# Kernel optimization log

Hardware: AMD Instinct MI355X
Metric: run time of the kernel (lower is better)

## Reference

```python
import jax, jax.numpy as jnp
import numpy as np
from jax import lax

H = 768            # encoder hidden size (bert-base)
NUM_LABELS = 3     # hardcoded in QNetwork.forward


def setup_inputs() -> dict:
    key = jax.random.key(0)
    ks = jax.random.split(key, 12)
    B, S1, S2 = 4, 256, 64
    s = 0.02
    f32 = jnp.float32
    return {
        "states": jax.random.normal(ks[0], (B, S1, H), f32),
        "state_mask": jnp.ones((B, S1), f32),
        "actions": jax.random.normal(ks[1], (B, S2, H), f32),
        "actions_mask": jnp.ones((B, S2), f32),
        # LSTM layer 0 (input h), layers 1-2 (input 2h); dirs stacked on axis 0
        "Wih0": jax.random.normal(ks[2], (2, 4 * H, H), f32) * s,
        "Whh0": jax.random.normal(ks[3], (2, 4 * H, H), f32) * s,
        "b0": jnp.zeros((2, 4 * H), f32),
        "Wih12": jax.random.normal(ks[4], (2, 2, 4 * H, 2 * H), f32) * s,
        "Whh12": jax.random.normal(ks[5], (2, 2, 4 * H, H), f32) * s,
        "b12": jnp.zeros((2, 2, 4 * H), f32),
        # AttentionLayer MLP: Linear(3h->h), ReLU, Linear(h->1)
        "attn_W1": jax.random.normal(ks[6], (H, 3 * H), f32) * s,
        "attn_b1": jnp.zeros((H,), f32),
        "attn_W2": jax.random.normal(ks[7], (1, H), f32) * s,
        "attn_b2": jnp.zeros((1,), f32),
        # dueling value head Linear(2h->1)
        "val_W": jax.random.normal(ks[8], (1, 2 * H), f32) * s,
        "val_b": jnp.zeros((1,), f32),
        # bilinear scoring weight [num_labels, h, 2h] and bias [num_labels]
        "weight": jax.random.normal(ks[9], (NUM_LABELS, H, 2 * H), f32) * s,
        "bias": jnp.zeros((NUM_LABELS,), f32),
    }


def _bilstm_layer(x, Wih, Whh, b):
    """x: [B,T,in]; Wih/Whh: [2,4h,*]; b: [2,4h] (b_ih+b_hh). Returns [B,T,2h]."""
    B = x.shape[0]
    Hh = Whh.shape[-1]
    xs = jnp.swapaxes(x, 0, 1)  # [T,B,in]
    outs = []
    for d, rev in ((0, False), (1, True)):
        Wi, Wh, bb = Wih[d], Whh[d], b[d]
        def step(carry, xt, Wi=Wi, Wh=Wh, bb=bb):
            h, c = carry
            g = xt @ Wi.T + h @ Wh.T + bb
            i, f, gg, o = jnp.split(g, 4, axis=-1)  # torch gate order i,f,g,o
            c = jax.nn.sigmoid(f) * c + jax.nn.sigmoid(i) * jnp.tanh(gg)
            h = jax.nn.sigmoid(o) * jnp.tanh(c)
            return (h, c), h
        init = (jnp.zeros((B, Hh), x.dtype), jnp.zeros((B, Hh), x.dtype))
        _, ys = lax.scan(step, init, xs, reverse=rev)
        outs.append(jnp.swapaxes(ys, 0, 1))
    return jnp.concatenate(outs, -1)


def _forward(states, state_mask, actions, actions_mask,
             Wih0, Whh0, b0, Wih12, Whh12, b12,
             attn_W1, attn_b1, attn_W2, attn_b2,
             val_W, val_b, weight, bias):
    # 3-layer bidirectional LSTM + tanh
    out = _bilstm_layer(states, Wih0, Whh0, b0)
    for l in range(2):
        out = _bilstm_layer(out, Wih12[l], Whh12[l], b12[l])
    out = jnp.tanh(out)  # [B,S1,2h]

    # AttentionLayer(query=actions, key=value=out, q_mask=actions_mask, k_mask=state_mask)
    # First linear on concat([q,k]) split into query/key parts to avoid materializing the 3h concat.
    W1q, W1k = attn_W1[:, :H], attn_W1[:, H:]
    hq = jnp.einsum('bqh,eh->bqe', actions, W1q)          # [B,S2,h]
    hk = jnp.einsum('bkh,eh->bke', out, W1k)              # [B,S1,h]
    h1 = jax.nn.relu(hq[:, :, None, :] + hk[:, None, :, :] + attn_b1)  # [B,S2,S1,h]
    scores = jnp.einsum('bqke,e->bqk', h1, attn_W2[0]) + attn_b2[0]    # [B,S2,S1]
    mask = actions_mask[:, :, None] * state_mask[:, None, :]
    A = jnp.exp(jnp.where(mask == 0, -jnp.inf, scores))
    A_sum = jnp.clip(jnp.sum(A, axis=-1, keepdims=True), 2e-15, None)
    states_feat = jnp.einsum('bqk,bkd->bqd', A / A_sum, out)  # [B,S2,2h]

    # masked mean over seq2 (aggregate='attn_mean')
    num = jnp.sum(actions_mask, axis=1)[:, None, None]
    state_semantic = jnp.sum(states_feat, axis=1, keepdims=True) / num  # [B,1,2h]

    # adv scores: sum_h actions[b,q,h] * (weight[l,h,d] states_feat[b,q,d])
    adv = jnp.einsum('lhd,bqd,bqh->bql', weight, states_feat, actions) + bias  # [B,S2,3]

    # dueling value head
    val = state_semantic @ val_W.T + val_b  # [B,1,1]
    q_value = val + adv - jnp.mean(adv, axis=(1, 2), keepdims=True)  # [B,S2,3]

    # actions_mask is all-ones so the nonzero-gather is the identity
    return q_value.reshape(-1, NUM_LABELS)


def reference(states, state_mask, actions, actions_mask,
              Wih0, Whh0, b0, Wih12, Whh12, b12,
              attn_W1, attn_b1, attn_W2, attn_b2,
              val_W, val_b, weight, bias):
    return _forward(states, state_mask, actions, actions_mask,
                    Wih0, Whh0, b0, Wih12, Whh12, b12,
                    attn_W1, attn_b1, attn_W2, attn_b2,
                    val_W, val_b, weight, bias)
```

## Files before the change

### kernel.cpp

```cpp
#include <hip/hip_runtime.h>

#define HD 768
#define G4 3072
#define T1 256
#define NS2 64
#define NL 3
#define NBLK_DIR 128
#define UPB 6

__device__ __forceinline__ float sigf(float x) { return 1.0f / (1.0f + expf(-x)); }

__device__ __forceinline__ void fence_vm() {
    asm volatile("s_waitcnt vmcnt(0)" ::: "memory");
}

__global__ __launch_bounds__(256) void gemm_f32(
    const float* __restrict__ A, int lda,
    const float* __restrict__ W, int ldw,
    const float* __restrict__ bias,
    float* __restrict__ C,
    int K, int n_per_chunk, long long chunk_stride)
{
    __shared__ __align__(16) float As[16 * 64];
    __shared__ __align__(16) float Ws[16 * 64];
    const int tid = threadIdx.x;
    const int tx = tid & 15, ty = tid >> 4;
    const int n0 = blockIdx.x * 64, m0 = blockIdx.y * 64;
    const int lr = tid >> 2, lc = tid & 3;

    float acc[4][4] = {{0.f}};
    const float* Ap = A + (size_t)(m0 + lr) * lda + lc * 4;
    const float* Wp = W + (size_t)(n0 + lr) * ldw + lc * 4;

    for (int k0 = 0; k0 < K; k0 += 16) {
        float4 av = *(const float4*)(Ap + k0);
        float4 wv = *(const float4*)(Wp + k0);
        __syncthreads();
        As[(lc * 4 + 0) * 64 + lr] = av.x;
        As[(lc * 4 + 1) * 64 + lr] = av.y;
        As[(lc * 4 + 2) * 64 + lr] = av.z;
        As[(lc * 4 + 3) * 64 + lr] = av.w;
        Ws[(lc * 4 + 0) * 64 + lr] = wv.x;
        Ws[(lc * 4 + 1) * 64 + lr] = wv.y;
        Ws[(lc * 4 + 2) * 64 + lr] = wv.z;
        Ws[(lc * 4 + 3) * 64 + lr] = wv.w;
        __syncthreads();
#pragma unroll
        for (int k = 0; k < 16; ++k) {
            float4 a = *(const float4*)&As[k * 64 + ty * 4];
            float4 b = *(const float4*)&Ws[k * 64 + tx * 4];
            float aa[4] = {a.x, a.y, a.z, a.w};
            float bb[4] = {b.x, b.y, b.z, b.w};
#pragma unroll
            for (int i = 0; i < 4; ++i)
#pragma unroll
                for (int j = 0; j < 4; ++j) acc[i][j] += aa[i] * bb[j];
        }
    }

    const int jg = n0 + tx * 4;
    const int chunk = jg / n_per_chunk;
    const int jo = jg - chunk * n_per_chunk;
    float4 bv = make_float4(0.f, 0.f, 0.f, 0.f);
    if (bias) bv = *(const float4*)&bias[jg];
    float* Cb = C + (size_t)chunk * chunk_stride + jo;
#pragma unroll
    for (int i = 0; i < 4; ++i) {
        const int m = m0 + ty * 4 + i;
        float4 o;
        o.x = acc[i][0] + bv.x;
        o.y = acc[i][1] + bv.y;
        o.z = acc[i][2] + bv.z;
        o.w = acc[i][3] + bv.w;
        *(float4*)&Cb[(size_t)m * n_per_chunk] = o;
    }
}

__global__ __launch_bounds__(256) void lstm_scan(
    const float* __restrict__ Whh,
    const float* __restrict__ G,
    float* __restrict__ Hout,
    float* __restrict__ hglob,
    unsigned* __restrict__ bar,
    int last)
{
    __shared__ __align__(16) float4 hs[960];
    __shared__ float gl[24 * 4];
    __shared__ float cst[24];
    const int tid = threadIdx.x;
    const int bid = blockIdx.x;
    const int dir = bid & 1;
    const int blkd = bid >> 1;
    const int u0 = blkd * UPB;

    const int ks = tid & 15, jp = tid >> 4;
    const bool act = (jp < 12);
    const bool kz = act && (ks == 0);

    const int r0 = 2 * jp, r1 = 2 * jp + 1;
    const int j0 = (r0 / 6) * HD + u0 + (r0 % 6);
    const int j1 = (r1 / 6) * HD + u0 + (r1 % 6);
    float4 w0[12], w1[12];
    if (act) {
        const float4* W4 = (const float4*)Whh + (size_t)dir * G4 * 192;
#pragma unroll
        for (int i = 0; i < 12; ++i) {
            w0[i] = W4[(size_t)j0 * 192 + i * 16 + ks];
            w1[i] = W4[(size_t)j1 * 192 + i * 16 + ks];
        }
    }
    if (tid < 24) cst[tid] = 0.f;

    unsigned* ctr = bar + dir * 256;
    unsigned* genp = bar + 512 + dir * 32;
    const size_t gdb = (size_t)dir * 4 * T1 * G4;
    const size_t bstr = (size_t)T1 * G4;
    float* hsf = (float*)hs;

    for (int s = 0; s < T1; ++s) {
        const int t = dir ? (T1 - 1 - s) : s;

        float gA[4], gB[4];
        if (kz) {
            const float* Gt = G + gdb + (size_t)t * G4;
#pragma unroll
            for (int b = 0; b < 4; ++b) {
                gA[b] = Gt[(size_t)b * bstr + j0];
                gB[b] = Gt[(size_t)b * bstr + j1];
            }
        }

        if (s == 0) {
#pragma unroll
            for (int r = 0; r < 3; ++r) {
                const int k = tid + 256 * r;
                hs[5 * (k >> 2) + (k & 3)] = make_float4(0.f, 0.f, 0.f, 0.f);
            }
        } else {
            const float* hp = hglob + ((size_t)((s & 1) * 2 + dir)) * HD * 4;
            float hv[12];
#pragma unroll
            for (int r = 0; r < 12; ++r)
                hv[r] = __hip_atomic_load(hp + tid + 256 * r, __ATOMIC_RELAXED,
                                          __HIP_MEMORY_SCOPE_AGENT);
#pragma unroll
            for (int r = 0; r < 12; ++r) {
                const int i = tid + 256 * r;
                const int k = i >> 2, b = i & 3;
                hsf[(5 * (k >> 2) + (k & 3)) * 4 + b] = hv[r];
            }
        }
        __syncthreads();

        if (act) {
            float4 a0 = make_float4(0.f, 0.f, 0.f, 0.f);
            float4 a1 = make_float4(0.f, 0.f, 0.f, 0.f);
#pragma unroll
            for (int i = 0; i < 12; ++i) {
                const int pb = 5 * (i * 16 + ks);
                const float4 h0 = hs[pb + 0];
                const float4 h1 = hs[pb + 1];
                const float4 h2 = hs[pb + 2];
                const float4 h3 = hs[pb + 3];
                const float4 wa = w0[i];
                const float4 wb = w1[i];
                a0.x += wa.x * h0.x; a0.y += wa.x * h0.y; a0.z += wa.x * h0.z; a0.w += wa.x * h0.w;
                a0.x += wa.y * h1.x; a0.y += wa.y * h1.y; a0.z += wa.y * h1.z; a0.w += wa.y * h1.w;
                a0.x += wa.z * h2.x; a0.y += wa.z * h2.y; a0.z += wa.z * h2.z; a0.w += wa.z * h2.w;
                a0.x += wa.w * h3.x; a0.y += wa.w * h3.y; a0.z += wa.w * h3.z; a0.w += wa.w * h3.w;
                a1.x += wb.x * h0.x; a1.y += wb.x * h0.y; a1.z += wb.x * h0.z; a1.w += wb.x * h0.w;
                a1.x += wb.y * h1.x; a1.y += wb.y * h1.y; a1.z += wb.y * h1.z; a1.w += wb.y * h1.w;
                a1.x += wb.z * h2.x; a1.y += wb.z * h2.y; a1.z += wb.z * h2.z; a1.w += wb.z * h2.w;
                a1.x += wb.w * h3.x; a1.y += wb.w * h3.y; a1.z += wb.w * h3.z; a1.w += wb.w * h3.w;
            }
#pragma unroll
            for (int off = 8; off; off >>= 1) {
                a0.x += __shfl_xor(a0.x, off);
                a0.y += __shfl_xor(a0.y, off);
                a0.z += __shfl_xor(a0.z, off);
                a0.w += __shfl_xor(a0.w, off);
                a1.x += __shfl_xor(a1.x, off);
                a1.y += __shfl_xor(a1.y, off);
                a1.z += __shfl_xor(a1.z, off);
                a1.w += __shfl_xor(a1.w, off);
            }
            if (ks == 0) {
                gl[r0 * 4 + 0] = a0.x + gA[0];
                gl[r0 * 4 + 1] = a0.y + gA[1];
                gl[r0 * 4 + 2] = a0.z + gA[2];
                gl[r0 * 4 + 3] = a0.w + gA[3];
                gl[r1 * 4 + 0] = a1.x + gB[0];
                gl[r1 * 4 + 1] = a1.y + gB[1];
                gl[r1 * 4 + 2] = a1.z + gB[2];
                gl[r1 * 4 + 3] = a1.w + gB[3];
            }
        }
        __syncthreads();

        if (tid < 24) {
            const int ui = tid >> 2, b = tid & 3;
            const float gi = gl[(0 * 6 + ui) * 4 + b];
            const float gf = gl[(1 * 6 + ui) * 4 + b];
            const float gg = gl[(2 * 6 + ui) * 4 + b];
            const float go = gl[(3 * 6 + ui) * 4 + b];
            const float c = sigf(gf) * cst[tid] + sigf(gi) * tanhf(gg);
            const float h = sigf(go) * tanhf(c);
            cst[tid] = c;
            __hip_atomic_store(
                &hglob[(((size_t)(((s + 1) & 1) * 2 + dir)) * HD + (u0 + ui)) * 4 + b],
                h, __ATOMIC_RELAXED, __HIP_MEMORY_SCOPE_AGENT);
            Hout[((size_t)b * T1 + t) * (2 * HD) + dir * HD + (u0 + ui)] =
                last ? tanhf(h) : h;
            fence_vm();
        }

        if (s < T1 - 1) {
            __syncthreads();
            if (tid == 0) {
                __hip_atomic_fetch_add(&ctr[(blkd & 7) * 32], 1u, __ATOMIC_RELAXED,
                                       __HIP_MEMORY_SCOPE_AGENT);
                const unsigned tgt = (unsigned)(NBLK_DIR * (s + 1));
                if (blkd == 0) {
                    for (;;) {
                        unsigned sum = 0;
#pragma unroll
                        for (int i = 0; i < 8; ++i)
                            sum += __hip_atomic_load(&ctr[i * 32], __ATOMIC_RELAXED,
                                                     __HIP_MEMORY_SCOPE_AGENT);
                        if (sum >= tgt) break;
                    }
                    __hip_atomic_store(genp, (unsigned)(s + 1), __ATOMIC_RELAXED,
                                       __HIP_MEMORY_SCOPE_AGENT);
                } else {
                    while (__hip_atomic_load(genp, __ATOMIC_RELAXED,
                                             __HIP_MEMORY_SCOPE_AGENT) <
                           (unsigned)(s + 1)) {}
                }
            }
            __syncthreads();
        }
    }
}

__global__ __launch_bounds__(256) void attn_kernel(
    const float* __restrict__ hq,
    const float* __restrict__ hk,
    const float* __restrict__ w2p,
    const float* __restrict__ b2p,
    const float* __restrict__ am,
    const float* __restrict__ sm,
    const float* __restrict__ H3,
    float* __restrict__ sf)
{
    __shared__ float hql[HD];
    __shared__ float w2[HD];
    __shared__ float Ash[T1];
    __shared__ float red[1];
    const int tid = threadIdx.x;
    const int bq = blockIdx.x;
    const int b = bq >> 6;

    for (int e = tid; e < HD; e += 256) {
        hql[e] = hq[(size_t)bq * HD + e];
        w2[e] = w2p[e];
    }
    __syncthreads();

    const int lane = tid & 63, wid = tid >> 6;
    const float amv = am[bq];
    const float b2 = b2p[0];
    for (int k = wid; k < T1; k += 4) {
        const float* hkp = hk + ((size_t)b * T1 + k) * HD;
        float s = 0.f;
#pragma unroll
        for (int i = 0; i < 12; ++i) {
            const int e = i * 64 + lane;
            float v = hql[e] + hkp[e];
            v = v > 0.f ? v : 0.f;
            s += v * w2[e];
        }
#pragma unroll
        for (int off = 32; off; off >>= 1) s += __shfl_xor(s, off);
        if (lane == 0) {
            const float m = amv * sm[b * T1 + k];
            Ash[k] = (m == 0.f) ? 0.f : expf(s + b2);
        }
    }
    __syncthreads();

    if (tid < 64) {
        float p = Ash[tid] + Ash[tid + 64] + Ash[tid + 128] + Ash[tid + 192];
#pragma unroll
        for (int off = 32; off; off >>= 1) p += __shfl_xor(p, off);
        if (tid == 0) red[0] = fmaxf(p, 2e-15f);
    }
    __syncthreads();
    const float inv = 1.f / red[0];

    for (int d = tid; d < 2 * HD; d += 256) {
        const float* hp = H3 + (size_t)b * T1 * 2 * HD + d;
        float acc = 0.f;
        for (int k = 0; k < T1; ++k) acc += Ash[k] * hp[(size_t)k * 2 * HD];
        sf[(size_t)bq * 2 * HD + d] = acc * inv;
    }
}

__global__ __launch_bounds__(256) void val_kernel(
    const float* __restrict__ sf, const float* __restrict__ am,
    const float* __restrict__ vw, const float* __restrict__ vb,
    float* __restrict__ val)
{
    __shared__ float red[4];
    const int b = blockIdx.x, tid = threadIdx.x;
    float num = 0.f;
    for (int q = 0; q < NS2; ++q) num += am[b * NS2 + q];
    float acc = 0.f;
    for (int d = tid; d < 2 * HD; d += 256) {
        float s = 0.f;
        for (int q = 0; q < NS2; ++q) s += sf[((size_t)(b * NS2 + q)) * 2 * HD + d];
        acc += (s / num) * vw[d];
    }
#pragma unroll
    for (int off = 32; off; off >>= 1) acc += __shfl_xor(acc, off);
    if ((tid & 63) == 0) red[tid >> 6] = acc;
    __syncthreads();
    if (tid == 0) val[b] = red[0] + red[1] + red[2] + red[3] + vb[0];
}

__global__ __launch_bounds__(256) void final_kernel(
    const float* __restrict__ Tb,
    const float* __restrict__ act,
    const float* __restrict__ bias,
    const float* __restrict__ val,
    float* __restrict__ out)
{
    __shared__ float adv[192];
    __shared__ float red[4];
    const int b = blockIdx.x, tid = threadIdx.x;
    const int lane = tid & 63, wid = tid >> 6;

    for (int idx = wid; idx < 192; idx += 4) {
        const int q = idx / 3, l = idx - q * 3;
        const float* tp = Tb + (size_t)l * T1 * HD + (size_t)(b * NS2 + q) * HD;
        const float* ap = act + (size_t)(b * NS2 + q) * HD;
        float s = 0.f;
#pragma unroll
        for (int i = 0; i < 12; ++i) {
            const int h = i * 64 + lane;
            s += tp[h] * ap[h];
        }
#pragma unroll
        for (int off = 32; off; off >>= 1) s += __shfl_xor(s, off);
        if (lane == 0) adv[idx] = s + bias[l];
    }
    __syncthreads();
    float part = (tid < 192) ? adv[tid] : 0.f;
#pragma unroll
    for (int off = 32; off; off >>= 1) part += __shfl_xor(part, off);
    if (lane == 0) red[wid] = part;
    __syncthreads();
    const float mean = (red[0] + red[1] + red[2] + red[3]) * (1.f / 192.f);
    const float vv = val[b];
    for (int idx = tid; idx < 192; idx += 256) {
        const int q = idx / 3, l = idx - q * 3;
        out[(size_t)(b * NS2 + q) * NL + l] = vv + adv[idx] - mean;
    }
}

extern "C" void kernel_launch(void* const* d_in, const int* in_sizes, int n_in,
                              void* d_out, int out_size, void* d_ws, size_t ws_size,
                              hipStream_t stream)
{
    const float* states = (const float*)d_in[0];
    const float* state_mask = (const float*)d_in[1];
    const float* actions = (const float*)d_in[2];
    const float* actions_mask = (const float*)d_in[3];
    const float* Wih0 = (const float*)d_in[4];
    const float* Whh0 = (const float*)d_in[5];
    const float* b0 = (const float*)d_in[6];
    const float* Wih12 = (const float*)d_in[7];
    const float* Whh12 = (const float*)d_in[8];
    const float* b12 = (const float*)d_in[9];
    const float* aW1 = (const float*)d_in[10];
    const float* ab1 = (const float*)d_in[11];
    const float* aW2 = (const float*)d_in[12];
    const float* ab2 = (const float*)d_in[13];
    const float* vW = (const float*)d_in[14];
    const float* vb = (const float*)d_in[15];
    const float* wgt = (const float*)d_in[16];
    const float* bias = (const float*)d_in[17];
    float* out = (float*)d_out;

    float* ws = (float*)d_ws;
    float* G = ws;
    float* B1 = G + 6291456;
    float* B2 = B1 + 1572864;
    float* hg = B2 + 1572864;
    unsigned* bar = (unsigned*)(hg + 12288);
    float* hq = G;
    float* hkb = G + 196608;
    float* sf = G + 983040;
    float* Tb = G + 1376256;
    float* val = G + 1966080;

    const dim3 blk(256);
    const long long gstride = (long long)4 * T1 * G4;

    hipMemsetAsync(bar, 0, 4096, stream);
    gemm_f32<<<dim3(6144 / 64, 1024 / 64), blk, 0, stream>>>(
        states, HD, Wih0, HD, b0, G, HD, G4, gstride);
    lstm_scan<<<dim3(256), blk, 0, stream>>>(Whh0, G, B1, hg, bar, 0);
    hipMemsetAsync(bar, 0, 4096, stream);
    gemm_f32<<<dim3(6144 / 64, 1024 / 64), blk, 0, stream>>>(
        B1, 2 * HD, Wih12, 2 * HD, b12, G, 2 * HD, G4, gstride);
    lstm_scan<<<dim3(256), blk, 0, stream>>>(Whh12, G, B2, hg, bar, 0);
    hipMemsetAsync(bar, 0, 4096, stream);
    gemm_f32<<<dim3(6144 / 64, 1024 / 64), blk, 0, stream>>>(
        B2, 2 * HD, Wih12 + (size_t)6144 * 1536, 2 * HD, b12 + 6144, G, 2 * HD, G4, gstride);
    lstm_scan<<<dim3(256), blk, 0, stream>>>(
        Whh12 + (size_t)2 * G4 * HD, G, B1, hg, bar, 1);
    gemm_f32<<<dim3(768 / 64, 256 / 64), blk, 0, stream>>>(
        actions, HD, aW1, 2304, ab1, hq, HD, HD, 0);
    gemm_f32<<<dim3(768 / 64, 1024 / 64), blk, 0, stream>>>(
        B1, 2 * HD, aW1 + 768, 2304, nullptr, hkb, 2 * HD, HD, 0);
    attn_kernel<<<dim3(256), blk, 0, stream>>>(hq, hkb, aW2, ab2, actions_mask,
                                               state_mask, B1, sf);
    val_kernel<<<dim3(4), blk, 0, stream>>>(sf, actions_mask, vW, vb, val);
    for (int l = 0; l < NL; ++l) {
        gemm_f32<<<dim3(768 / 64, 256 / 64), blk, 0, stream>>>(
            sf, 2 * HD, wgt + (size_t)l * HD * 2 * HD, 2 * HD, nullptr,
            Tb + (size_t)l * T1 * HD, 2 * HD, HD, 0);
    }
    final_kernel<<<dim3(4), blk, 0, stream>>>(Tb, actions, bias, val, out);
}
```

Measured before the change: 4.280 ms.

## Replace LSTM grid barrier with per-block tagged cache-line flags

The per-step grid-wide barrier in the persistent LSTM scan (counter fetch-add, a master block polling, then a generation broadcast) is removed. Each block now writes its 24 hidden values plus a step tag into its own 128-byte line. Consumers spin on each producer line's tag before reading it, which cuts the two-hop barrier latency. The next step's input-gate loads are also prefetched after publishing h, so they overlap the wait. The tag store relies on vmcnt(0) ordering rather than release semantics, which is a memory-ordering risk.

New measurement: 5.279 ms. 23.4% more time.

```diff
diff --git a/kernel.cpp b/kernel.cpp
--- a/kernel.cpp
+++ b/kernel.cpp
@@ -80,8 +80,7 @@
     const float* __restrict__ Whh,
     const float* __restrict__ G,
     float* __restrict__ Hout,
-    float* __restrict__ hglob,
-    unsigned* __restrict__ bar,
+    float* __restrict__ hline,
     int last)
 {
     __shared__ __align__(16) float4 hs[960];
@@ -97,6 +96,9 @@
     const bool act = (jp < 12);
     const bool kz = act && (ks == 0);
 
+    const int cline = tid >> 1;
+    const int chalf = tid & 1;
+
     const int r0 = 2 * jp, r1 = 2 * jp + 1;
     const int j0 = (r0 / 6) * HD + u0 + (r0 % 6);
     const int j1 = (r1 / 6) * HD + u0 + (r1 % 6);
@@ -111,24 +113,23 @@
     }
     if (tid < 24) cst[tid] = 0.f;
 
-    unsigned* ctr = bar + dir * 256;
-    unsigned* genp = bar + 512 + dir * 32;
     const size_t gdb = (size_t)dir * 4 * T1 * G4;
     const size_t bstr = (size_t)T1 * G4;
     float* hsf = (float*)hs;
 
+    float gA[4], gB[4];
+    if (kz) {
+        const int t0 = dir ? (T1 - 1) : 0;
+        const float* Gt = G + gdb + (size_t)t0 * G4;
+#pragma unroll
+        for (int b = 0; b < 4; ++b) {
+            gA[b] = Gt[(size_t)b * bstr + j0];
+            gB[b] = Gt[(size_t)b * bstr + j1];
+        }
+    }
+
     for (int s = 0; s < T1; ++s) {
         const int t = dir ? (T1 - 1 - s) : s;
-
-        float gA[4], gB[4];
-        if (kz) {
-            const float* Gt = G + gdb + (size_t)t * G4;
-#pragma unroll
-            for (int b = 0; b < 4; ++b) {
-                gA[b] = Gt[(size_t)b * bstr + j0];
-                gB[b] = Gt[(size_t)b * bstr + j1];
-            }
-        }
 
         if (s == 0) {
 #pragma unroll
@@ -137,17 +138,18 @@
                 hs[5 * (k >> 2) + (k & 3)] = make_float4(0.f, 0.f, 0.f, 0.f);
             }
         } else {
-            const float* hp = hglob + ((size_t)((s & 1) * 2 + dir)) * HD * 4;
-            float hv[12];
-#pragma unroll
-            for (int r = 0; r < 12; ++r)
-                hv[r] = __hip_atomic_load(hp + tid + 256 * r, __ATOMIC_RELAXED,
-                                          __HIP_MEMORY_SCOPE_AGENT);
-#pragma unroll
-            for (int r = 0; r < 12; ++r) {
-                const int i = tid + 256 * r;
-                const int k = i >> 2, b = i & 3;
-                hsf[(5 * (k >> 2) + (k & 3)) * 4 + b] = hv[r];
+            const float* base =
+                hline + (((size_t)((s & 1) * 2 + dir)) * 128 + cline) * 32;
+            const unsigned* tagp = (const unsigned*)(base + 24);
+            while (__hip_atomic_load(tagp, __ATOMIC_RELAXED,
+                                     __HIP_MEMORY_SCOPE_AGENT) < (unsigned)s) {}
+#pragma unroll
+            for (int j = 0; j < 12; ++j) {
+                const int d = chalf * 12 + j;
+                const float v = __hip_atomic_load(base + d, __ATOMIC_RELAXED,
+                                                  __HIP_MEMORY_SCOPE_AGENT);
+                const int k = cline * 6 + (d >> 2);
+                hsf[(5 * (k >> 2) + (k & 3)) * 4 + (d & 3)] = v;
             }
         }
         __syncthreads();
@@ -197,6 +199,9 @@
         }
         __syncthreads();
 
+        float hval = 0.f;
+        float* wline =
+            hline + (((size_t)(((s + 1) & 1) * 2 + dir)) * 128 + blkd) * 32;
         if (tid < 24) {
             const int ui = tid >> 2, b = tid & 3;
             const float gi = gl[(0 * 6 + ui) * 4 + b];
@@ -204,40 +209,33 @@
             const float gg = gl[(2 * 6 + ui) * 4 + b];
             const float go = gl[(3 * 6 + ui) * 4 + b];
             const float c = sigf(gf) * cst[tid] + sigf(gi) * tanhf(gg);
-            const float h = sigf(go) * tanhf(c);
+            hval = sigf(go) * tanhf(c);
             cst[tid] = c;
-            __hip_atomic_store(
-                &hglob[(((size_t)(((s + 1) & 1) * 2 + dir)) * HD + (u0 + ui)) * 4 + b],
-                h, __ATOMIC_RELAXED, __HIP_MEMORY_SCOPE_AGENT);
+            if (s < T1 - 1) {
+                __hip_atomic_store(wline + tid, hval, __ATOMIC_RELAXED,
+                                   __HIP_MEMORY_SCOPE_AGENT);
+            }
+        }
+        if (s < T1 - 1) {
+            if (tid < 64) fence_vm();
+            if (tid == 0) {
+                __hip_atomic_store((unsigned*)(wline + 24), (unsigned)(s + 1),
+                                   __ATOMIC_RELAXED, __HIP_MEMORY_SCOPE_AGENT);
+            }
+        }
+        if (tid < 24) {
+            const int ui = tid >> 2, b = tid & 3;
             Hout[((size_t)b * T1 + t) * (2 * HD) + dir * HD + (u0 + ui)] =
-                last ? tanhf(h) : h;
-            fence_vm();
-        }
-
-        if (s < T1 - 1) {
-            __syncthreads();
-            if (tid == 0) {
-                __hip_atomic_fetch_add(&ctr[(blkd & 7) * 32], 1u, __ATOMIC_RELAXED,
-                                       __HIP_MEMORY_SCOPE_AGENT);
-                const unsigned tgt = (unsigned)(NBLK_DIR * (s + 1));
-                if (blkd == 0) {
-                    for (;;) {
-                        unsigned sum = 0;
-#pragma unroll
-                        for (int i = 0; i < 8; ++i)
-                            sum += __hip_atomic_load(&ctr[i * 32], __ATOMIC_RELAXED,
-                                                     __HIP_MEMORY_SCOPE_AGENT);
-                        if (sum >= tgt) break;
-                    }
-                    __hip_atomic_store(genp, (unsigned)(s + 1), __ATOMIC_RELAXED,
-                                       __HIP_MEMORY_SCOPE_AGENT);
-                } else {
-                    while (__hip_atomic_load(genp, __ATOMIC_RELAXED,
-                                             __HIP_MEMORY_SCOPE_AGENT) <
-                           (unsigned)(s + 1)) {}
-                }
-            }
-            __syncthreads();
+                last ? tanhf(hval) : hval;
+        }
+        if (s < T1 - 1 && kz) {
+            const int tn = dir ? (T1 - 2 - s) : (s + 1);
+            const float* Gt = G + gdb + (size_t)tn * G4;
+#pragma unroll
+            for (int b = 0; b < 4; ++b) {
+                gA[b] = Gt[(size_t)b * bstr + j0];
+                gB[b] = Gt[(size_t)b * bstr + j1];
+            }
         }
     }
 }
@@ -395,8 +393,7 @@
     float* G = ws;
     float* B1 = G + 6291456;
     float* B2 = B1 + 1572864;
-    float* hg = B2 + 1572864;
-    unsigned* bar = (unsigned*)(hg + 12288);
+    float* hline = B2 + 1572864;
     float* hq = G;
     float* hkb = G + 196608;
     float* sf = G + 983040;
@@ -406,19 +403,19 @@
     const dim3 blk(256);
     const long long gstride = (long long)4 * T1 * G4;
 
-    hipMemsetAsync(bar, 0, 4096, stream);
+    hipMemsetAsync(hline, 0, 65536, stream);
     gemm_f32<<<dim3(6144 / 64, 1024 / 64), blk, 0, stream>>>(
         states, HD, Wih0, HD, b0, G, HD, G4, gstride);
-    lstm_scan<<<dim3(256), blk, 0, stream>>>(Whh0, G, B1, hg, bar, 0);
-    hipMemsetAsync(bar, 0, 4096, stream);
+    lstm_scan<<<dim3(256), blk, 0, stream>>>(Whh0, G, B1, hline, 0);
+    hipMemsetAsync(hline, 0, 65536, stream);
     gemm_f32<<<dim3(6144 / 64, 1024 / 64), blk, 0, stream>>>(
         B1, 2 * HD, Wih12, 2 * HD, b12, G, 2 * HD, G4, gstride);
-    lstm_scan<<<dim3(256), blk, 0, stream>>>(Whh12, G, B2, hg, bar, 0);
-    hipMemsetAsync(bar, 0, 4096, stream);
+    lstm_scan<<<dim3(256), blk, 0, stream>>>(Whh12, G, B2, hline, 0);
+    hipMemsetAsync(hline, 0, 65536, stream);
     gemm_f32<<<dim3(6144 / 64, 1024 / 64), blk, 0, stream>>>(
         B2, 2 * HD, Wih12 + (size_t)6144 * 1536, 2 * HD, b12 + 6144, G, 2 * HD, G4, gstride);
     lstm_scan<<<dim3(256), blk, 0, stream>>>(
-        Whh12 + (size_t)2 * G4 * HD, G, B1, hg, bar, 1);
+        Whh12 + (size_t)2 * G4 * HD, G, B1, hline, 1);
     gemm_f32<<<dim3(768 / 64, 256 / 64), blk, 0, stream>>>(
         actions, HD, aW1, 2304, ab1, hq, HD, HD, 0);
     gemm_f32<<<dim3(768 / 64, 1024 / 64), blk, 0, stream>>>(
```

## Double-buffer GEMM shared tiles and shorten LSTM step barrier critical path

Applied to the files above, without the earlier changes.

The input-projection GEMM now uses two shared-memory buffers and prefetches the next K-slice into registers while computing the current one, which removes one __syncthreads per iteration. In the recurrent LSTM kernel, the grid-barrier counter increment now happens right after the h-state stores are fenced within the first wavefront, before the Hout write, and the block-wide __syncthreads before the barrier is dropped. This shortens each time step's serial critical path. The shuffle reduction loop is also restructured, and the relaxed ordering between the h stores, the fence and the counter increment depends on every h-writing thread sitting in wave 0.

New measurement: 4.296 ms. Within noise of the previous version (+0.4%).

```diff
diff --git a/kernel.cpp b/kernel.cpp
--- a/kernel.cpp
+++ b/kernel.cpp
@@ -21,8 +21,8 @@
     float* __restrict__ C,
     int K, int n_per_chunk, long long chunk_stride)
 {
-    __shared__ __align__(16) float As[16 * 64];
-    __shared__ __align__(16) float Ws[16 * 64];
+    __shared__ __align__(16) float As[2][16 * 64];
+    __shared__ __align__(16) float Ws[2][16 * 64];
     const int tid = threadIdx.x;
     const int tx = tid & 15, ty = tid >> 4;
     const int n0 = blockIdx.x * 64, m0 = blockIdx.y * 64;
@@ -32,23 +32,29 @@
     const float* Ap = A + (size_t)(m0 + lr) * lda + lc * 4;
     const float* Wp = W + (size_t)(n0 + lr) * ldw + lc * 4;
 
+    float4 av = *(const float4*)(Ap);
+    float4 wv = *(const float4*)(Wp);
+    int cur = 0;
     for (int k0 = 0; k0 < K; k0 += 16) {
-        float4 av = *(const float4*)(Ap + k0);
-        float4 wv = *(const float4*)(Wp + k0);
+        float* Asb = As[cur];
+        float* Wsb = Ws[cur];
+        Asb[(lc * 4 + 0) * 64 + lr] = av.x;
+        Asb[(lc * 4 + 1) * 64 + lr] = av.y;
+        Asb[(lc * 4 + 2) * 64 + lr] = av.z;
+        Asb[(lc * 4 + 3) * 64 + lr] = av.w;
+        Wsb[(lc * 4 + 0) * 64 + lr] = wv.x;
+        Wsb[(lc * 4 + 1) * 64 + lr] = wv.y;
+        Wsb[(lc * 4 + 2) * 64 + lr] = wv.z;
+        Wsb[(lc * 4 + 3) * 64 + lr] = wv.w;
         __syncthreads();
-        As[(lc * 4 + 0) * 64 + lr] = av.x;
-        As[(lc * 4 + 1) * 64 + lr] = av.y;
-        As[(lc * 4 + 2) * 64 + lr] = av.z;
-        As[(lc * 4 + 3) * 64 + lr] = av.w;
-        Ws[(lc * 4 + 0) * 64 + lr] = wv.x;
-        Ws[(lc * 4 + 1) * 64 + lr] = wv.y;
-        Ws[(lc * 4 + 2) * 64 + lr] = wv.z;
-        Ws[(lc * 4 + 3) * 64 + lr] = wv.w;
-        __syncthreads();
+        if (k0 + 16 < K) {
+            av = *(const float4*)(Ap + k0 + 16);
+            wv = *(const float4*)(Wp + k0 + 16);
+        }
 #pragma unroll
         for (int k = 0; k < 16; ++k) {
-            float4 a = *(const float4*)&As[k * 64 + ty * 4];
-            float4 b = *(const float4*)&Ws[k * 64 + tx * 4];
+            float4 a = *(const float4*)&Asb[k * 64 + ty * 4];
+            float4 b = *(const float4*)&Wsb[k * 64 + tx * 4];
             float aa[4] = {a.x, a.y, a.z, a.w};
             float bb[4] = {b.x, b.y, b.z, b.w};
 #pragma unroll
@@ -56,6 +62,7 @@
 #pragma unroll
                 for (int j = 0; j < 4; ++j) acc[i][j] += aa[i] * bb[j];
         }
+        cur ^= 1;
     }
 
     const int jg = n0 + tx * 4;
@@ -174,7 +181,19 @@
                 a1.x += wb.w * h3.x; a1.y += wb.w * h3.y; a1.z += wb.w * h3.z; a1.w += wb.w * h3.w;
             }
 #pragma unroll
-            for (int off = 8; off; off >>= 1) {
+            for (int off = 8; off; off <<= 1) {
+                a0.x += __shfl_xor(a0.x, off);
+                a0.y += __shfl_xor(a0.y, off);
+                a0.z += __shfl_xor(a0.z, off);
+                a0.w += __shfl_xor(a0.w, off);
+                a1.x += __shfl_xor(a1.x, off);
+                a1.y += __shfl_xor(a1.y, off);
+                a1.z += __shfl_xor(a1.z, off);
+                a1.w += __shfl_xor(a1.w, off);
+                if (off == 8) break;
+            }
+#pragma unroll
+            for (int off = 1; off < 8; off <<= 1) {
                 a0.x += __shfl_xor(a0.x, off);
                 a0.y += __shfl_xor(a0.y, off);
                 a0.z += __shfl_xor(a0.z, off);
@@ -197,6 +216,7 @@
         }
         __syncthreads();
 
+        float hval = 0.f;
         if (tid < 24) {
             const int ui = tid >> 2, b = tid & 3;
             const float gi = gl[(0 * 6 + ui) * 4 + b];
@@ -204,21 +224,25 @@
             const float gg = gl[(2 * 6 + ui) * 4 + b];
             const float go = gl[(3 * 6 + ui) * 4 + b];
             const float c = sigf(gf) * cst[tid] + sigf(gi) * tanhf(gg);
-            const float h = sigf(go) * tanhf(c);
+            hval = sigf(go) * tanhf(c);
             cst[tid] = c;
             __hip_atomic_store(
                 &hglob[(((size_t)(((s + 1) & 1) * 2 + dir)) * HD + (u0 + ui)) * 4 + b],
-                h, __ATOMIC_RELAXED, __HIP_MEMORY_SCOPE_AGENT);
+                hval, __ATOMIC_RELAXED, __HIP_MEMORY_SCOPE_AGENT);
+        }
+        if (tid < 64) fence_vm();
+        if (s < T1 - 1 && tid == 0) {
+            __hip_atomic_fetch_add(&ctr[(blkd & 7) * 32], 1u, __ATOMIC_RELAXED,
+                                   __HIP_MEMORY_SCOPE_AGENT);
+        }
+        if (tid < 24) {
+            const int ui = tid >> 2, b = tid & 3;
             Hout[((size_t)b * T1 + t) * (2 * HD) + dir * HD + (u0 + ui)] =
-                last ? tanhf(h) : h;
-            fence_vm();
+                last ? tanhf(hval) : hval;
         }
 
         if (s < T1 - 1) {
-            __syncthreads();
             if (tid == 0) {
-                __hip_atomic_fetch_add(&ctr[(blkd & 7) * 32], 1u, __ATOMIC_RELAXED,
-                                       __HIP_MEMORY_SCOPE_AGENT);
                 const unsigned tgt = (unsigned)(NBLK_DIR * (s + 1));
                 if (blkd == 0) {
                     for (;;) {
```
